# Kernel optimization log

Hardware: AMD Instinct MI355X
Metric: run time of the kernel (lower is better)

The kernel has to match this reference:

```python
import jax, jax.numpy as jnp
import numpy as np

EPS = 1e-7  # tf.keras.backend.epsilon()


def squash(v, axis=-1):
    s = jnp.sum(jnp.square(v), axis=axis, keepdims=True)
    scale = s / (1.0 + s) / jnp.sqrt(s + EPS)
    return scale * v


def setup_inputs() -> dict:
    key = jax.random.key(0)
    k1, k2 = jax.random.split(key)
    B, I, D = 64, 2048, 16   # batch, input_num_capsule, input_dim_capsule
    J, K = 32, 16            # num_capsule, dim_capsule
    inputs = jax.random.normal(k1, (B, I, D), dtype=jnp.float32)
    # glorot_uniform-ish init for W: [in_caps, num_caps, in_dim, dim_caps]
    limit = np.sqrt(6.0 / (D + K)).astype(np.float32)
    W = jax.random.uniform(k2, (I, J, D, K), dtype=jnp.float32, minval=-limit, maxval=limit)
    return {"inputs": inputs, "W": W}


def reference(inputs, W, routings=3):
    # u_hat[b,i,j,:] = inputs[b,i,:] @ W[i,j,:,:]
    u_hat = jnp.einsum('bid,ijdk->bijk', inputs, W)  # [B, I, J, K]
    B, I, J, _ = u_hat.shape
    b = jnp.zeros((B, I, J, 1), dtype=u_hat.dtype)
    outputs = None
    for r in range(routings):
        c = jax.nn.softmax(b, axis=2)                              # [B, I, J, 1]
        outputs = squash(jnp.sum(c * u_hat, axis=1, keepdims=True))  # [B, 1, J, K]
        if r < routings - 1:
            b = b + jnp.sum(u_hat * outputs, axis=-1, keepdims=True)
    return jnp.squeeze(outputs, axis=1)  # [B, J, K]
```

## Files before the change

kernel.cpp:

```cpp
#include <hip/hip_runtime.h>
#include <hip/hip_bf16.h>


#define B_ 64
#define I_ 2048
#define D_ 16
#define J_ 32
#define K_ 16
#define JK 512
#define NBLK 256
#define GI 8

typedef __attribute__((ext_vector_type(8))) short short8;
typedef __attribute__((ext_vector_type(4))) float float4v;

__device__ __forceinline__ unsigned short f2bf(float f) {
    union { float f; unsigned int i; } v;
    v.f = f;
    const unsigned int x = v.i;
    return (unsigned short)((x + 0x7fffu + ((x >> 16) & 1u)) >> 16);
}

__device__ __forceinline__ void bar_lds() {
    asm volatile("s_waitcnt lgkmcnt(0)\n\ts_barrier" ::: "memory");
}

template <int MODE>
__global__ __launch_bounds__(512)
void caps_pass(const float* __restrict__ x, const float* __restrict__ W,
               const float* __restrict__ vsum, float* __restrict__ part) {
    __shared__ unsigned short wlds[2][32 * 384];
    __shared__ unsigned short zbuf[8];
    __shared__ float ebuf[2][4][2][16];
    const int tid = threadIdx.x;
    const int lane = tid & 63;
    const int wv = tid >> 6;
    const int bt = wv & 3;
    const int jh = wv >> 2;
    const int quad = lane >> 4;
    const int l15 = lane & 15;
    const int b = bt * 16 + l15;
    const int i0 = blockIdx.x * GI;

    if (tid < 8) zbuf[tid] = 0;

    float4 vv[16];
    if (MODE == 1) {
#pragma unroll
        for (int jj = 0; jj < 16; ++jj)
            vv[jj] = reinterpret_cast<const float4*>(
                vsum + b * JK + (jh * 16 + jj) * 16 + quad * 4)[0];
    }

    float4 acc2[16];
#pragma unroll
    for (int jj = 0; jj < 16; ++jj) {
        acc2[jj].x = 0.f; acc2[jj].y = 0.f;
        acc2[jj].z = 0.f; acc2[jj].w = 0.f;
    }

    const int sk = tid & 15;
    const int sj = tid >> 4;
    const float* wp = W + (size_t)i0 * (J_ * D_ * K_) + sj * (D_ * K_) + sk;
    const float* xp = x + ((size_t)b * I_ + i0) * D_ + (quad & 1) * 8;

    float vals[16];
#pragma unroll
    for (int d = 0; d < 16; ++d) vals[d] = wp[d * K_];
    float4 xr0 = reinterpret_cast<const float4*>(xp)[0];
    float4 xr1 = reinterpret_cast<const float4*>(xp)[1];
    {
        unsigned int pk[8];
#pragma unroll
        for (int q = 0; q < 8; ++q)
            pk[q] = ((unsigned int)f2bf(vals[2 * q + 1]) << 16) |
                    f2bf(vals[2 * q]);
        uint4* dst = reinterpret_cast<uint4*>(&wlds[0][sj * 384 + sk * 24]);
        uint4 w0; w0.x = pk[0]; w0.y = pk[1]; w0.z = pk[2]; w0.w = pk[3];
        uint4 w1; w1.x = pk[4]; w1.y = pk[5]; w1.z = pk[6]; w1.w = pk[7];
        dst[0] = w0; dst[1] = w1;
    }

    for (int t = 0; t < GI; ++t) {
        const int p = t & 1;

        bar_lds();

        float nv[16];
        float4 nx0, nx1;
        if (t < GI - 1) {
            const float* wn = wp + (size_t)(t + 1) * (J_ * D_ * K_);
#pragma unroll
            for (int d = 0; d < 16; ++d) nv[d] = wn[d * K_];
            const float* xn = xp + (t + 1) * D_;
            nx0 = reinterpret_cast<const float4*>(xn)[0];
            nx1 = reinterpret_cast<const float4*>(xn)[1];
        }

        union { uint4 u; short8 s; } bfrag;
        bfrag.u.x = ((unsigned int)f2bf(xr0.y) << 16) | f2bf(xr0.x);
        bfrag.u.y = ((unsigned int)f2bf(xr0.w) << 16) | f2bf(xr0.z);
        bfrag.u.z = ((unsigned int)f2bf(xr1.y) << 16) | f2bf(xr1.x);
        bfrag.u.w = ((unsigned int)f2bf(xr1.w) << 16) | f2bf(xr1.z);
        if (quad >= 2) { bfrag.u.x = 0; bfrag.u.y = 0; bfrag.u.z = 0; bfrag.u.w = 0; }

        const unsigned short* aptr =
            (quad >= 2) ? zbuf : (&wlds[p][0] + l15 * 24 + (quad & 1) * 8);
        const int astride = (quad >= 2) ? 0 : 384;

        if (MODE == 0) {
#pragma unroll
            for (int jj = 0; jj < 16; ++jj) {
                const int j = jh * 16 + jj;
                union { uint4 u; short8 s; } af;
                af.u = *reinterpret_cast<const uint4*>(aptr + (size_t)j * astride);
                float4v a = {0.f, 0.f, 0.f, 0.f};
                a = __builtin_amdgcn_mfma_f32_16x16x32_bf16(af.s, bfrag.s, a,
                                                            0, 0, 0);
                acc2[jj].x += a[0]; acc2[jj].y += a[1];
                acc2[jj].z += a[2]; acc2[jj].w += a[3];
            }
        } else {
            float e[16];
            float E = 0.f;
#pragma unroll
            for (int jj = 0; jj < 16; ++jj) {
                const int j = jh * 16 + jj;
                union { uint4 u; short8 s; } af;
                af.u = *reinterpret_cast<const uint4*>(aptr + (size_t)j * astride);
                float4v a = {0.f, 0.f, 0.f, 0.f};
                a = __builtin_amdgcn_mfma_f32_16x16x32_bf16(af.s, bfrag.s, a,
                                                            0, 0, 0);
                float pj = a[0] * vv[jj].x + a[1] * vv[jj].y +
                           a[2] * vv[jj].z + a[3] * vv[jj].w;
                pj += __shfl_xor(pj, 16, 64);
                pj += __shfl_xor(pj, 32, 64);
                const float ee = __expf(pj);
                e[jj] = ee;
                E += ee;
            }
            if (quad == 0) ebuf[p][bt][jh][l15] = E;
            bar_lds();
            const float S = E + ebuf[p][bt][1 - jh][l15];
            const float r = __builtin_amdgcn_rcpf(S);
#pragma unroll
            for (int jj = 0; jj < 16; ++jj) {
                const int j = jh * 16 + jj;
                union { uint4 u; short8 s; } af;
                af.u = *reinterpret_cast<const uint4*>(aptr + (size_t)j * astride);
                float4v a = {0.f, 0.f, 0.f, 0.f};
                a = __builtin_amdgcn_mfma_f32_16x16x32_bf16(af.s, bfrag.s, a,
                                                            0, 0, 0);
                const float c = e[jj] * r;
                acc2[jj].x += c * a[0]; acc2[jj].y += c * a[1];
                acc2[jj].z += c * a[2]; acc2[jj].w += c * a[3];
            }
        }

        if (t < GI - 1) {
            unsigned int pk[8];
#pragma unroll
            for (int q = 0; q < 8; ++q)
                pk[q] = ((unsigned int)f2bf(nv[2 * q + 1]) << 16) |
                        f2bf(nv[2 * q]);
            uint4* dst =
                reinterpret_cast<uint4*>(&wlds[p ^ 1][sj * 384 + sk * 24]);
            uint4 w0; w0.x = pk[0]; w0.y = pk[1]; w0.z = pk[2]; w0.w = pk[3];
            uint4 w1; w1.x = pk[4]; w1.y = pk[5]; w1.z = pk[6]; w1.w = pk[7];
            dst[0] = w0; dst[1] = w1;
            xr0 = nx0; xr1 = nx1;
        }
    }

    float* pp = part + ((size_t)blockIdx.x * B_ + b) * JK + jh * 256 + quad * 4;
#pragma unroll
    for (int jj = 0; jj < 16; ++jj)
        reinterpret_cast<float4*>(pp + jj * 16)[0] = acc2[jj];
}

template <int MODE>
__global__ __launch_bounds__(512)
void caps_squashN(const float* __restrict__ part, float* __restrict__ vsum,
                  float* __restrict__ out) {
    __shared__ float red[3][128];
    const int bl = blockIdx.x >> 2;
    const int q4 = blockIdx.x & 3;
    const int jk128 = threadIdx.x & 127;
    const int h = threadIdx.x >> 7;
    const int jk = q4 * 128 + jk128;

    float s = 0.f;
#pragma unroll 8
    for (int p = h * (NBLK / 4); p < (h + 1) * (NBLK / 4); ++p)
        s += part[((size_t)p * B_ + bl) * JK + jk];

    if (h > 0) red[h - 1][jk128] = s;
    __syncthreads();
    if (h == 0) {
        s += red[0][jk128] + red[1][jk128] + red[2][jk128];
        if (MODE == 0) s *= (1.f / 32.f);
        float qq = s * s;
        qq += __shfl_xor(qq, 1, 64);
        qq += __shfl_xor(qq, 2, 64);
        qq += __shfl_xor(qq, 4, 64);
        qq += __shfl_xor(qq, 8, 64);
        const float scale = qq / ((1.f + qq) * sqrtf(qq + 1e-7f));
        const float v = scale * s;
        if (MODE == 0)      vsum[bl * JK + jk] = v;
        else if (MODE == 1) vsum[bl * JK + jk] += v;
        else                out[(size_t)bl * JK + jk] = v;
    }
}

extern "C" void kernel_launch(void* const* d_in, const int* in_sizes, int n_in,
                              void* d_out, int out_size, void* d_ws,
                              size_t ws_size, hipStream_t stream) {
    const float* x = (const float*)d_in[0];
    const float* W = (const float*)d_in[1];
    float* out = (float*)d_out;

    char* ws = (char*)d_ws;
    float* part = (float*)ws;
    float* vsum =
        (float*)(ws + (size_t)B_ * I_ * JK * 2 + (size_t)64 * B_ * JK * 4);

    caps_pass<0><<<NBLK, 512, 0, stream>>>(x, W, nullptr, part);
    caps_squashN<0><<<B_ * 4, 512, 0, stream>>>(part, vsum, nullptr);
    caps_pass<1><<<NBLK, 512, 0, stream>>>(x, W, vsum, part);
    caps_squashN<1><<<B_ * 4, 512, 0, stream>>>(part, vsum, nullptr);
    caps_pass<1><<<NBLK, 512, 0, stream>>>(x, W, vsum, part);
    caps_squashN<2><<<B_ * 4, 512, 0, stream>>>(part, vsum, out);
}
```

Measured before the change: 192.8 us.

## Switch to 32x32x16 MFMA with single-buffered W and LDS-transposed partial stores

Replaces the 16x16x32 MFMA tiles, half of which were zero-padded, with 32x32x16 bf16 MFMAs, so each wave handles 32 batches by 8 capsules. In routing passes u_hat is computed once per step and reused for both the logits and the weighted accumulation, instead of issuing the MFMAs twice. The W staging buffer becomes single-buffered with an extra barrier per step. Partials are transposed through a dynamic LDS buffer of about 132 KB so global writes are coalesced in batch-major order, and the reduce kernel is updated to match. The large LDS request limits occupancy to one block per CU, and x loads are no longer prefetched.

```diff
diff --git a/kernel.cpp b/kernel.cpp
--- a/kernel.cpp
+++ b/kernel.cpp
@@ -12,7 +12,9 @@
 #define GI 8
 
 typedef __attribute__((ext_vector_type(8))) short short8;
-typedef __attribute__((ext_vector_type(4))) float float4v;
+typedef __attribute__((ext_vector_type(16))) float float16v;
+
+#define SMEM_BYTES 135168
 
 __device__ __forceinline__ unsigned short f2bf(float f) {
     union { float f; unsigned int i; } v;
@@ -29,132 +31,137 @@
 __global__ __launch_bounds__(512)
 void caps_pass(const float* __restrict__ x, const float* __restrict__ W,
                const float* __restrict__ vsum, float* __restrict__ part) {
-    __shared__ unsigned short wlds[2][32 * 384];
-    __shared__ unsigned short zbuf[8];
-    __shared__ float ebuf[2][4][2][16];
+    extern __shared__ char smem[];
+    unsigned short* wlds = (unsigned short*)smem;
+    float* ebuf = (float*)(smem + 24576);
+    float* ct = (float*)smem;
+
     const int tid = threadIdx.x;
     const int lane = tid & 63;
-    const int wv = tid >> 6;
-    const int bt = wv & 3;
-    const int jh = wv >> 2;
-    const int quad = lane >> 4;
-    const int l15 = lane & 15;
-    const int b = bt * 16 + l15;
+    const int w = tid >> 6;
+    const int bt = w & 1;
+    const int jg = w >> 1;
+    const int l31 = lane & 31;
+    const int h = lane >> 5;
+    const int b = bt * 32 + l31;
     const int i0 = blockIdx.x * GI;
 
-    if (tid < 8) zbuf[tid] = 0;
-
-    float4 vv[16];
+    float4 vv[4][2][2];
     if (MODE == 1) {
 #pragma unroll
-        for (int jj = 0; jj < 16; ++jj)
-            vv[jj] = reinterpret_cast<const float4*>(
-                vsum + b * JK + (jh * 16 + jj) * 16 + quad * 4)[0];
-    }
-
-    float4 acc2[16];
-#pragma unroll
-    for (int jj = 0; jj < 16; ++jj) {
-        acc2[jj].x = 0.f; acc2[jj].y = 0.f;
-        acc2[jj].z = 0.f; acc2[jj].w = 0.f;
-    }
-
+        for (int m = 0; m < 4; ++m)
+#pragma unroll
+            for (int jp = 0; jp < 2; ++jp) {
+                const float* vp =
+                    vsum + b * JK + (jg * 8 + m * 2 + jp) * 16 + 4 * h;
+                vv[m][jp][0] = reinterpret_cast<const float4*>(vp)[0];
+                vv[m][jp][1] = reinterpret_cast<const float4*>(vp + 8)[0];
+            }
+    }
+
+    float16v acc[4];
+#pragma unroll
+    for (int m = 0; m < 4; ++m)
+#pragma unroll
+        for (int r = 0; r < 16; ++r) acc[m][r] = 0.f;
+
+    const int sj = tid >> 4;
     const int sk = tid & 15;
-    const int sj = tid >> 4;
     const float* wp = W + (size_t)i0 * (J_ * D_ * K_) + sj * (D_ * K_) + sk;
-    const float* xp = x + ((size_t)b * I_ + i0) * D_ + (quad & 1) * 8;
-
-    float vals[16];
-#pragma unroll
-    for (int d = 0; d < 16; ++d) vals[d] = wp[d * K_];
-    float4 xr0 = reinterpret_cast<const float4*>(xp)[0];
-    float4 xr1 = reinterpret_cast<const float4*>(xp)[1];
+
     {
+        float vals[16];
+#pragma unroll
+        for (int d = 0; d < 16; ++d) vals[d] = wp[d * K_];
         unsigned int pk[8];
 #pragma unroll
         for (int q = 0; q < 8; ++q)
             pk[q] = ((unsigned int)f2bf(vals[2 * q + 1]) << 16) |
                     f2bf(vals[2 * q]);
-        uint4* dst = reinterpret_cast<uint4*>(&wlds[0][sj * 384 + sk * 24]);
+        uint4* dst = reinterpret_cast<uint4*>(wlds + (sj * 16 + sk) * 24);
         uint4 w0; w0.x = pk[0]; w0.y = pk[1]; w0.z = pk[2]; w0.w = pk[3];
         uint4 w1; w1.x = pk[4]; w1.y = pk[5]; w1.z = pk[6]; w1.w = pk[7];
         dst[0] = w0; dst[1] = w1;
     }
 
+    const int abase = ((jg * 8 + (l31 >> 4)) * 16 + (lane & 15)) * 24 + h * 8;
+    const float* xbase = x + (size_t)b * I_ * D_ + h * 8;
+
     for (int t = 0; t < GI; ++t) {
-        const int p = t & 1;
-
+        const int i = i0 + t;
         bar_lds();
 
         float nv[16];
-        float4 nx0, nx1;
         if (t < GI - 1) {
             const float* wn = wp + (size_t)(t + 1) * (J_ * D_ * K_);
 #pragma unroll
             for (int d = 0; d < 16; ++d) nv[d] = wn[d * K_];
-            const float* xn = xp + (t + 1) * D_;
-            nx0 = reinterpret_cast<const float4*>(xn)[0];
-            nx1 = reinterpret_cast<const float4*>(xn)[1];
         }
 
         union { uint4 u; short8 s; } bfrag;
-        bfrag.u.x = ((unsigned int)f2bf(xr0.y) << 16) | f2bf(xr0.x);
-        bfrag.u.y = ((unsigned int)f2bf(xr0.w) << 16) | f2bf(xr0.z);
-        bfrag.u.z = ((unsigned int)f2bf(xr1.y) << 16) | f2bf(xr1.x);
-        bfrag.u.w = ((unsigned int)f2bf(xr1.w) << 16) | f2bf(xr1.z);
-        if (quad >= 2) { bfrag.u.x = 0; bfrag.u.y = 0; bfrag.u.z = 0; bfrag.u.w = 0; }
-
-        const unsigned short* aptr =
-            (quad >= 2) ? zbuf : (&wlds[p][0] + l15 * 24 + (quad & 1) * 8);
-        const int astride = (quad >= 2) ? 0 : 384;
+        {
+            const float* xp = xbase + (size_t)i * D_;
+            const float4 x0 = reinterpret_cast<const float4*>(xp)[0];
+            const float4 x1 = reinterpret_cast<const float4*>(xp)[1];
+            bfrag.u.x = ((unsigned int)f2bf(x0.y) << 16) | f2bf(x0.x);
+            bfrag.u.y = ((unsigned int)f2bf(x0.w) << 16) | f2bf(x0.z);
+            bfrag.u.z = ((unsigned int)f2bf(x1.y) << 16) | f2bf(x1.x);
+            bfrag.u.w = ((unsigned int)f2bf(x1.w) << 16) | f2bf(x1.z);
+        }
+
+        float16v u[4];
+#pragma unroll
+        for (int m = 0; m < 4; ++m) {
+            union { uint4 q; short8 s; } af;
+            af.q = *reinterpret_cast<const uint4*>(wlds + abase + m * 768);
+            float16v z;
+#pragma unroll
+            for (int r = 0; r < 16; ++r) z[r] = 0.f;
+            u[m] = __builtin_amdgcn_mfma_f32_32x32x16_bf16(af.s, bfrag.s, z,
+                                                           0, 0, 0);
+        }
 
         if (MODE == 0) {
 #pragma unroll
-            for (int jj = 0; jj < 16; ++jj) {
-                const int j = jh * 16 + jj;
-                union { uint4 u; short8 s; } af;
-                af.u = *reinterpret_cast<const uint4*>(aptr + (size_t)j * astride);
-                float4v a = {0.f, 0.f, 0.f, 0.f};
-                a = __builtin_amdgcn_mfma_f32_16x16x32_bf16(af.s, bfrag.s, a,
-                                                            0, 0, 0);
-                acc2[jj].x += a[0]; acc2[jj].y += a[1];
-                acc2[jj].z += a[2]; acc2[jj].w += a[3];
-            }
+            for (int m = 0; m < 4; ++m) acc[m] += u[m];
+            bar_lds();
         } else {
-            float e[16];
+            float e[4][2];
             float E = 0.f;
 #pragma unroll
-            for (int jj = 0; jj < 16; ++jj) {
-                const int j = jh * 16 + jj;
-                union { uint4 u; short8 s; } af;
-                af.u = *reinterpret_cast<const uint4*>(aptr + (size_t)j * astride);
-                float4v a = {0.f, 0.f, 0.f, 0.f};
-                a = __builtin_amdgcn_mfma_f32_16x16x32_bf16(af.s, bfrag.s, a,
-                                                            0, 0, 0);
-                float pj = a[0] * vv[jj].x + a[1] * vv[jj].y +
-                           a[2] * vv[jj].z + a[3] * vv[jj].w;
-                pj += __shfl_xor(pj, 16, 64);
-                pj += __shfl_xor(pj, 32, 64);
-                const float ee = __expf(pj);
-                e[jj] = ee;
-                E += ee;
-            }
-            if (quad == 0) ebuf[p][bt][jh][l15] = E;
+            for (int m = 0; m < 4; ++m)
+#pragma unroll
+                for (int jp = 0; jp < 2; ++jp) {
+                    const int rb = jp * 8;
+                    float p = u[m][rb + 0] * vv[m][jp][0].x +
+                              u[m][rb + 1] * vv[m][jp][0].y +
+                              u[m][rb + 2] * vv[m][jp][0].z +
+                              u[m][rb + 3] * vv[m][jp][0].w +
+                              u[m][rb + 4] * vv[m][jp][1].x +
+                              u[m][rb + 5] * vv[m][jp][1].y +
+                              u[m][rb + 6] * vv[m][jp][1].z +
+                              u[m][rb + 7] * vv[m][jp][1].w;
+                    p += __shfl_xor(p, 32, 64);
+                    const float ee = __expf(p);
+                    e[m][jp] = ee;
+                    E += ee;
+                }
+            if (h == 0) ebuf[(((t & 1) * 2 + bt) * 4 + jg) * 32 + l31] = E;
             bar_lds();
-            const float S = E + ebuf[p][bt][1 - jh][l15];
-            const float r = __builtin_amdgcn_rcpf(S);
-#pragma unroll
-            for (int jj = 0; jj < 16; ++jj) {
-                const int j = jh * 16 + jj;
-                union { uint4 u; short8 s; } af;
-                af.u = *reinterpret_cast<const uint4*>(aptr + (size_t)j * astride);
-                float4v a = {0.f, 0.f, 0.f, 0.f};
-                a = __builtin_amdgcn_mfma_f32_16x16x32_bf16(af.s, bfrag.s, a,
-                                                            0, 0, 0);
-                const float c = e[jj] * r;
-                acc2[jj].x += c * a[0]; acc2[jj].y += c * a[1];
-                acc2[jj].z += c * a[2]; acc2[jj].w += c * a[3];
-            }
+            float Et = 0.f;
+#pragma unroll
+            for (int g = 0; g < 4; ++g)
+                Et += ebuf[(((t & 1) * 2 + bt) * 4 + g) * 32 + l31];
+            const float r = __builtin_amdgcn_rcpf(Et);
+#pragma unroll
+            for (int m = 0; m < 4; ++m)
+#pragma unroll
+                for (int jp = 0; jp < 2; ++jp) {
+                    const float c = e[m][jp] * r;
+#pragma unroll
+                    for (int q = 0; q < 8; ++q)
+                        acc[m][jp * 8 + q] += c * u[m][jp * 8 + q];
+                }
         }
 
         if (t < GI - 1) {
@@ -163,19 +170,46 @@
             for (int q = 0; q < 8; ++q)
                 pk[q] = ((unsigned int)f2bf(nv[2 * q + 1]) << 16) |
                         f2bf(nv[2 * q]);
-            uint4* dst =
-                reinterpret_cast<uint4*>(&wlds[p ^ 1][sj * 384 + sk * 24]);
+            uint4* dst = reinterpret_cast<uint4*>(wlds + (sj * 16 + sk) * 24);
             uint4 w0; w0.x = pk[0]; w0.y = pk[1]; w0.z = pk[2]; w0.w = pk[3];
             uint4 w1; w1.x = pk[4]; w1.y = pk[5]; w1.z = pk[6]; w1.w = pk[7];
             dst[0] = w0; dst[1] = w1;
-            xr0 = nx0; xr1 = nx1;
-        }
-    }
-
-    float* pp = part + ((size_t)blockIdx.x * B_ + b) * JK + jh * 256 + quad * 4;
-#pragma unroll
-    for (int jj = 0; jj < 16; ++jj)
-        reinterpret_cast<float4*>(pp + jj * 16)[0] = acc2[jj];
+        }
+    }
+
+    bar_lds();
+    {
+        float* cw = ct + w * (32 * 132);
+#pragma unroll
+        for (int m = 0; m < 4; ++m)
+#pragma unroll
+            for (int jp = 0; jp < 2; ++jp) {
+                const int col = (m * 2 + jp) * 16 + 4 * h;
+                float4 v0, v1;
+                v0.x = acc[m][jp * 8 + 0]; v0.y = acc[m][jp * 8 + 1];
+                v0.z = acc[m][jp * 8 + 2]; v0.w = acc[m][jp * 8 + 3];
+                v1.x = acc[m][jp * 8 + 4]; v1.y = acc[m][jp * 8 + 5];
+                v1.z = acc[m][jp * 8 + 6]; v1.w = acc[m][jp * 8 + 7];
+                *reinterpret_cast<float4*>(cw + l31 * 132 + col) = v0;
+                *reinterpret_cast<float4*>(cw + l31 * 132 + col + 8) = v1;
+            }
+    }
+    bar_lds();
+    {
+        const int bb = tid >> 3;
+        const int oct = tid & 7;
+        float* gp = part + ((size_t)bb * NBLK + blockIdx.x) * JK + oct * 64;
+#pragma unroll
+        for (int s = 0; s < 4; ++s) {
+            const int j = oct * 4 + s;
+            const float* src = ct + ((bb >> 5) + 2 * (j >> 3)) * (32 * 132) +
+                               (bb & 31) * 132 + (j & 7) * 16;
+#pragma unroll
+            for (int q = 0; q < 4; ++q)
+                reinterpret_cast<float4*>(gp + s * 16 + q * 4)[0] =
+                    reinterpret_cast<const float4*>(src + q * 4)[0];
+        }
+    }
 }
 
 template <int MODE>
@@ -192,7 +226,7 @@
     float s = 0.f;
 #pragma unroll 8
     for (int p = h * (NBLK / 4); p < (h + 1) * (NBLK / 4); ++p)
-        s += part[((size_t)p * B_ + bl) * JK + jk];
+        s += part[((size_t)bl * NBLK + p) * JK + jk];
 
     if (h > 0) red[h - 1][jk128] = s;
     __syncthreads();
@@ -224,10 +258,10 @@
     float* vsum =
         (float*)(ws + (size_t)B_ * I_ * JK * 2 + (size_t)64 * B_ * JK * 4);
 
-    caps_pass<0><<<NBLK, 512, 0, stream>>>(x, W, nullptr, part);
+    caps_pass<0><<<NBLK, 512, SMEM_BYTES, stream>>>(x, W, nullptr, part);
     caps_squashN<0><<<B_ * 4, 512, 0, stream>>>(part, vsum, nullptr);
-    caps_pass<1><<<NBLK, 512, 0, stream>>>(x, W, vsum, part);
+    caps_pass<1><<<NBLK, 512, SMEM_BYTES, stream>>>(x, W, vsum, part);
     caps_squashN<1><<<B_ * 4, 512, 0, stream>>>(part, vsum, nullptr);
-    caps_pass<1><<<NBLK, 512, 0, stream>>>(x, W, vsum, part);
+    caps_pass<1><<<NBLK, 512, SMEM_BYTES, stream>>>(x, W, vsum, part);
     caps_squashN<2><<<B_ * 4, 512, 0, stream>>>(part, vsum, out);
 }
```

Result: no change. 195.0 us (+1.1%).

## Relayout partial sums and split reduction into two-stage redA/redB kernels

Applied to the files above, without the earlier changes.

The per-block partial outputs are now stored in a j-pair-major, b-contiguous layout, so the cross-block reduction reads contiguous float4 chunks. The single squash reduction kernel becomes two kernels: a 256-block first stage that sums 16 partials each, and a 16-block second stage that finishes the sum and applies squash through shared memory. This targets the strided, poorly parallel reduction reads. In exchange it adds an extra launch per routing iteration, scattered scalar stores of the stride-64 partials, and a second stage that runs on only 16 blocks.

```diff
diff --git a/kernel.cpp b/kernel.cpp
--- a/kernel.cpp
+++ b/kernel.cpp
@@ -10,6 +10,7 @@
 #define JK 512
 #define NBLK 256
 #define GI 8
+#define MB(n) ((size_t)(n) << 20)
 
 typedef __attribute__((ext_vector_type(8))) short short8;
 typedef __attribute__((ext_vector_type(4))) float float4v;
@@ -172,43 +173,74 @@
         }
     }
 
-    float* pp = part + ((size_t)blockIdx.x * B_ + b) * JK + jh * 256 + quad * 4;
-#pragma unroll
-    for (int jj = 0; jj < 16; ++jj)
-        reinterpret_cast<float4*>(pp + jj * 16)[0] = acc2[jj];
+#pragma unroll
+    for (int jj = 0; jj < 16; ++jj) {
+        const int jq = jh * 8 + (jj >> 1);
+        float* gp = part + ((size_t)jq * NBLK + blockIdx.x) * 2048 +
+                    (jj & 1) * 1024 + b;
+        gp[(quad * 4 + 0) * 64] = acc2[jj].x;
+        gp[(quad * 4 + 1) * 64] = acc2[jj].y;
+        gp[(quad * 4 + 2) * 64] = acc2[jj].z;
+        gp[(quad * 4 + 3) * 64] = acc2[jj].w;
+    }
+}
+
+__global__ __launch_bounds__(512)
+void caps_redA(const float* __restrict__ part, float* __restrict__ part2) {
+    const int jq = blockIdx.x >> 4, pb = blockIdx.x & 15;
+    const int e4 = threadIdx.x * 4;
+    float4 s = {0.f, 0.f, 0.f, 0.f};
+#pragma unroll 4
+    for (int icb = 0; icb < 16; ++icb) {
+        const float4 v = *reinterpret_cast<const float4*>(
+            part + ((size_t)jq * NBLK + pb * 16 + icb) * 2048 + e4);
+        s.x += v.x; s.y += v.y; s.z += v.z; s.w += v.w;
+    }
+    *reinterpret_cast<float4*>(part2 + ((size_t)jq * 16 + pb) * 2048 + e4) = s;
 }
 
 template <int MODE>
 __global__ __launch_bounds__(512)
-void caps_squashN(const float* __restrict__ part, float* __restrict__ vsum,
-                  float* __restrict__ out) {
-    __shared__ float red[3][128];
-    const int bl = blockIdx.x >> 2;
-    const int q4 = blockIdx.x & 3;
-    const int jk128 = threadIdx.x & 127;
-    const int h = threadIdx.x >> 7;
-    const int jk = q4 * 128 + jk128;
-
-    float s = 0.f;
-#pragma unroll 8
-    for (int p = h * (NBLK / 4); p < (h + 1) * (NBLK / 4); ++p)
-        s += part[((size_t)p * B_ + bl) * JK + jk];
-
-    if (h > 0) red[h - 1][jk128] = s;
+void caps_redB(const float* __restrict__ part2, float* __restrict__ vsum,
+               float* __restrict__ out) {
+    __shared__ float sq[2048];
+    __shared__ float sc[128];
+    const int jq = blockIdx.x;
+    const int tid = threadIdx.x;
+    const int e4 = tid * 4;
+    float4 s = {0.f, 0.f, 0.f, 0.f};
+#pragma unroll
+    for (int pb = 0; pb < 16; ++pb) {
+        const float4 v = *reinterpret_cast<const float4*>(
+            part2 + ((size_t)jq * 16 + pb) * 2048 + e4);
+        s.x += v.x; s.y += v.y; s.z += v.z; s.w += v.w;
+    }
+    if (MODE == 0) {
+        s.x *= (1.f / 32.f); s.y *= (1.f / 32.f);
+        s.z *= (1.f / 32.f); s.w *= (1.f / 32.f);
+    }
+    *reinterpret_cast<float4*>(&sq[e4]) = s;
     __syncthreads();
-    if (h == 0) {
-        s += red[0][jk128] + red[1][jk128] + red[2][jk128];
-        if (MODE == 0) s *= (1.f / 32.f);
-        float qq = s * s;
-        qq += __shfl_xor(qq, 1, 64);
-        qq += __shfl_xor(qq, 2, 64);
-        qq += __shfl_xor(qq, 4, 64);
-        qq += __shfl_xor(qq, 8, 64);
-        const float scale = qq / ((1.f + qq) * sqrtf(qq + 1e-7f));
-        const float v = scale * s;
-        if (MODE == 0)      vsum[bl * JK + jk] = v;
-        else if (MODE == 1) vsum[bl * JK + jk] += v;
-        else                out[(size_t)bl * JK + jk] = v;
+    if (tid < 128) {
+        const int j1 = tid >> 6, bb = tid & 63;
+        float nn = 0.f;
+#pragma unroll
+        for (int k = 0; k < 16; ++k) {
+            const float v = sq[j1 * 1024 + k * 64 + bb];
+            nn += v * v;
+        }
+        sc[tid] = nn / ((1.f + nn) * sqrtf(nn + 1e-7f));
+    }
+    __syncthreads();
+#pragma unroll
+    for (int q = 0; q < 4; ++q) {
+        const int e = e4 + q;
+        const int j1 = e >> 10, k = (e >> 6) & 15, bb = e & 63;
+        const float v = sq[e] * sc[j1 * 64 + bb];
+        const int j = jq * 2 + j1;
+        if (MODE == 0)      vsum[(size_t)bb * JK + j * 16 + k] = v;
+        else if (MODE == 1) vsum[(size_t)bb * JK + j * 16 + k] += v;
+        else                out[(size_t)bb * JK + j * 16 + k] = v;
     }
 }
 
@@ -221,13 +253,16 @@
 
     char* ws = (char*)d_ws;
     float* part = (float*)ws;
-    float* vsum =
-        (float*)(ws + (size_t)B_ * I_ * JK * 2 + (size_t)64 * B_ * JK * 4);
+    float* part2 = (float*)(ws + MB(36));
+    float* vsum = (float*)(ws + MB(40));
 
     caps_pass<0><<<NBLK, 512, 0, stream>>>(x, W, nullptr, part);
-    caps_squashN<0><<<B_ * 4, 512, 0, stream>>>(part, vsum, nullptr);
+    caps_redA<<<256, 512, 0, stream>>>(part, part2);
+    caps_redB<0><<<16, 512, 0, stream>>>(part2, vsum, nullptr);
     caps_pass<1><<<NBLK, 512, 0, stream>>>(x, W, vsum, part);
-    caps_squashN<1><<<B_ * 4, 512, 0, stream>>>(part, vsum, nullptr);
+    caps_redA<<<256, 512, 0, stream>>>(part, part2);
+    caps_redB<1><<<16, 512, 0, stream>>>(part2, vsum, nullptr);
     caps_pass<1><<<NBLK, 512, 0, stream>>>(x, W, vsum, part);
-    caps_squashN<2><<<B_ * 4, 512, 0, stream>>>(part, vsum, out);
-}
+    caps_redA<<<256, 512, 0, stream>>>(part, part2);
+    caps_redB<2><<<16, 512, 0, stream>>>(part2, vsum, out);
+}
```

Measured after the change: 204.0 us. 5.8% more time.
